# Performance work log

Measured on AMD Instinct MI355X. Metric: run time of the kernel, lower is better.

Reference implementation:

```python
import jax, jax.numpy as jnp
import numpy as np

N, E, G, H, L, GD = 100000, 1600000, 64, 128, 3, 32
NEG_SLOPE = 0.2
EPS = 1e-5


def setup_inputs() -> dict:
    key = jax.random.key(0)
    ks = jax.random.split(key, 10)
    s = 1.0 / np.sqrt(H)
    return {
        "x": jax.random.normal(ks[0], (N, H), jnp.float32),
        "global_feat": jax.random.normal(ks[1], (G, GD), jnp.float32),
        "W_src": jax.random.normal(ks[2], (L, H, H), jnp.float32) * s,
        "W_dst": jax.random.normal(ks[3], (L, H, H), jnp.float32) * s,
        "att": jax.random.normal(ks[4], (L, H), jnp.float32) * s,
        "b_conv": jnp.zeros((L, H), jnp.float32),
        "gn_w": jnp.ones((L, H), jnp.float32),
        "gn_b": jnp.zeros((L, H), jnp.float32),
        "gn_ms": jnp.ones((L, H), jnp.float32),
        "W1": jax.random.normal(ks[5], (H * L + GD, H), jnp.float32) * (1.0 / np.sqrt(H * L + GD)),
        "b1": jnp.zeros((H,), jnp.float32),
        "W2": jax.random.normal(ks[6], (H, 1), jnp.float32) * s,
        "b2": jnp.zeros((1,), jnp.float32),
        "edge_index": jax.random.randint(ks[7], (2, E), 0, N, jnp.int64),
        "batch": jnp.sort(jax.random.randint(ks[8], (N,), 0, G, jnp.int64)),
    }


def reference(x, global_feat, W_src, W_dst, att, b_conv, gn_w, gn_b, gn_ms,
              W1, b1, W2, b2, edge_index, batch):
    n = x.shape[0]
    g = global_feat.shape[0]
    layers = W_src.shape[0]
    loops = jnp.arange(n, dtype=edge_index.dtype)
    src = jnp.concatenate([edge_index[0], loops])  # add_self_loops=True
    dst = jnp.concatenate([edge_index[1], loops])
    counts = jnp.maximum(
        jax.ops.segment_sum(jnp.ones((n,), x.dtype), batch, num_segments=g), 1.0)

    outs = []
    for l in range(layers):
        # --- GATv2Conv (heads=1) ---
        xl = x @ W_src[l]          # source transform [N,H]
        xr = x @ W_dst[l]          # target transform [N,H]
        e = jax.nn.leaky_relu(xl[src] + xr[dst], NEG_SLOPE) @ att[l]  # [Etot]
        emax = jax.ops.segment_max(e, dst, num_segments=n)
        ex = jnp.exp(e - emax[dst])
        denom = jax.ops.segment_sum(ex, dst, num_segments=n)
        alpha = ex / denom[dst]
        h = jax.ops.segment_sum(alpha[:, None] * xl[src], dst, num_segments=n) + b_conv[l]
        # --- GraphNorm ---
        mean = jax.ops.segment_sum(h, batch, num_segments=g) / counts[:, None]
        sub = h - gn_ms[l] * mean[batch]
        var = jax.ops.segment_sum(sub * sub, batch, num_segments=g) / counts[:, None]
        h = gn_w[l] * sub * jax.lax.rsqrt(var[batch] + EPS) + gn_b[l]
        x = jax.nn.relu(h)
        # --- global_mean_pool ---
        outs.append(jax.ops.segment_sum(x, batch, num_segments=g) / counts[:, None])

    hcat = jnp.concatenate(outs + [global_feat], axis=1)  # JK cat + global feats
    z = jax.nn.relu(hcat @ W1 + b1)  # dropout = identity (eval)
    return z @ W2 + b2
```

## Files before the change

### kernel.cpp

```cpp
#include <hip/hip_runtime.h>
#include <hip/hip_bf16.h>
#include <math.h>

#define N_    100000
#define E_    1600000
#define ETOT_ 1700000
#define G_    64
#define H_    128
#define GH_   8192
#define L_    3
#define GD_   32
#define NEG_  0.2f
#define EPS_  1e-5f

#define NBUK_ 391
#define CH_   2048
#define MCH_  782

typedef unsigned short ushort_t;
typedef unsigned int uint_t;
typedef __attribute__((ext_vector_type(4))) float f32x4;
typedef __attribute__((ext_vector_type(8))) short bf16x8;
typedef __attribute__((ext_vector_type(8))) unsigned short ushort8;

__device__ __forceinline__ ushort_t bfb(float f) {
    __hip_bfloat16 h = __float2bfloat16(f);
    return *reinterpret_cast<ushort_t*>(&h);
}
__device__ __forceinline__ float uf(ushort_t u) {
    return __uint_as_float(((uint_t)u) << 16);
}


__global__ void k_init(float* pooled, float* gsum, float* gsq, int* gstart,
                       const int* __restrict__ batch) {
    int i = blockIdx.x * 256 + threadIdx.x;
    if (i < L_ * GH_) { pooled[i] = 0.f; gsum[i] = 0.f; gsq[i] = 0.f; }
    if (i <= G_) {
        int lo = 0, hi = N_;
        while (lo < hi) { int mid = (lo + hi) >> 1; if (batch[mid] < i) lo = mid + 1; else hi = mid; }
        gstart[i] = lo;
    }
}


__global__ __launch_bounds__(256) void k_bcount(const int* __restrict__ edst, int* __restrict__ C) {
    __shared__ int hist[NBUK_];
    int t = threadIdx.x, m = blockIdx.x;
    for (int i = t; i < NBUK_; i += 256) hist[i] = 0;
    __syncthreads();
    int base = m * CH_;
#pragma unroll
    for (int j = 0; j < CH_ / 256; j++) {
        int e = base + j * 256 + t;
        if (e < E_) atomicAdd(&hist[edst[e] >> 8], 1);
    }
    __syncthreads();
    for (int i = t; i < NBUK_; i += 256) C[i * MCH_ + m] = hist[i];
}

__global__ __launch_bounds__(1024) void k_bscan(int* __restrict__ C, int* __restrict__ bucketEdges) {
    __shared__ int arr[1024];
    int b = blockIdx.x, t = threadIdx.x;
    int v = (t < MCH_) ? C[b * MCH_ + t] : 0;
    arr[t] = v;
    __syncthreads();
    for (int off = 1; off < 1024; off <<= 1) {
        int x = (t >= off) ? arr[t - off] : 0;
        __syncthreads();
        arr[t] += x;
        __syncthreads();
    }
    if (t < MCH_) C[b * MCH_ + t] = arr[t] - v;
    if (t == 1023) bucketEdges[b] = arr[1023];
}

__global__ __launch_bounds__(512) void k_bscan2(const int* __restrict__ bucketEdges,
                                                int* __restrict__ bstartE, int* __restrict__ bstartT,
                                                int* __restrict__ rowptr) {
    __shared__ int aE[512], aT[512];
    int t = threadIdx.x;
    int e = 0, tot = 0;
    if (t < NBUK_) {
        e = bucketEdges[t];
        int nib = N_ - t * 256; if (nib > 256) nib = 256;
        tot = e + nib;
    }
    aE[t] = e; aT[t] = tot;
    __syncthreads();
    for (int off = 1; off < 512; off <<= 1) {
        int xe = (t >= off) ? aE[t - off] : 0;
        int xt = (t >= off) ? aT[t - off] : 0;
        __syncthreads();
        aE[t] += xe; aT[t] += xt;
        __syncthreads();
    }
    if (t < NBUK_) { bstartE[t] = aE[t] - e; bstartT[t] = aT[t] - tot; }
    if (t == 0) rowptr[N_] = ETOT_;
}

__global__ __launch_bounds__(256) void k_bscatter(const int* __restrict__ esrc, const int* __restrict__ edst,
                                                  const int* __restrict__ C, const int* __restrict__ bstartE,
                                                  int2* __restrict__ stag) {
    __shared__ int cur[NBUK_];
    int t = threadIdx.x, m = blockIdx.x;
    for (int i = t; i < NBUK_; i += 256) cur[i] = C[i * MCH_ + m] + bstartE[i];
    __syncthreads();
    int base = m * CH_;
#pragma unroll
    for (int j = 0; j < CH_ / 256; j++) {
        int e = base + j * 256 + t;
        if (e < E_) {
            int s = esrc[e], d = edst[e];
            int pos = atomicAdd(&cur[d >> 8], 1);
            int2 p; p.x = s; p.y = d;
            stag[pos] = p;
        }
    }
}

__global__ __launch_bounds__(256) void k_bfinal(const int2* __restrict__ stag,
                                                const int* __restrict__ bucketEdges,
                                                const int* __restrict__ bstartE, const int* __restrict__ bstartT,
                                                int* __restrict__ rowptr, int* __restrict__ colarr) {
    __shared__ int deg[256];
    __shared__ int cursor[256];
    int b = blockIdx.x, t = threadIdx.x;
    int nb0 = b * 256;
    int nib = N_ - nb0; if (nib > 256) nib = 256;
    int ebeg = bstartE[b], ecnt = bucketEdges[b];
    deg[t] = (t < nib) ? 1 : 0;
    __syncthreads();
    for (int i = t; i < ecnt; i += 256) {
        int2 p = stag[ebeg + i];
        atomicAdd(&deg[p.y - nb0], 1);
    }
    __syncthreads();
    int v = deg[t];
    cursor[t] = v;
    __syncthreads();
    for (int off = 1; off < 256; off <<= 1) {
        int x = (t >= off) ? cursor[t - off] : 0;
        __syncthreads();
        cursor[t] += x;
        __syncthreads();
    }
    int excl = cursor[t] - v;
    int rowbase = bstartT[b];
    if (t < nib) {
        rowptr[nb0 + t] = rowbase + excl;
        colarr[rowbase + excl] = nb0 + t;
    }
    __syncthreads();
    cursor[t] = excl + 1;
    __syncthreads();
    for (int i = t; i < ecnt; i += 256) {
        int2 p = stag[ebeg + i];
        int pos = atomicAdd(&cursor[p.y - nb0], 1);
        colarr[rowbase + pos] = p.x;
    }
}


__global__ void k_prep_w(const float* __restrict__ Ws, const float* __restrict__ Wd,
                         ushort_t* __restrict__ Wt) {
    int i = blockIdx.x * 256 + threadIdx.x;
    if (i >= L_ * 256 * H_) return;
    int l = i >> 15;
    int r = i & 32767;
    int c = r >> 7, k = r & 127;
    float v = (c < H_) ? Ws[(size_t)l * H_ * H_ + k * H_ + c]
                       : Wd[(size_t)l * H_ * H_ + k * H_ + (c - H_)];
    Wt[i] = bfb(v);
}


template<int FIRST>
__global__ __launch_bounds__(256) void k_mfma_t(const float* __restrict__ x0,
                                                const ushort_t* __restrict__ hin,
                                                const int* __restrict__ batch,
                                                const float* __restrict__ mv,
                                                const float* __restrict__ iv,
                                                const float* __restrict__ bb,
                                                const ushort_t* __restrict__ Wt,
                                                ushort_t* __restrict__ xlb,
                                                ushort_t* __restrict__ xrb) {
    int wv = threadIdx.x >> 6, lane = threadIdx.x & 63;
    int row0 = (blockIdx.x * 4 + wv) * 16;
    if (row0 >= N_) return;
    int sl = lane & 15, q = lane >> 4;
    int row = row0 + sl;

    bf16x8 a[4];
    if (FIRST) {
        const float* ap = x0 + (size_t)row * H_ + q * 8;
#pragma unroll
        for (int kk = 0; kk < 4; kk++) {
            float4 v0 = *(const float4*)(ap + kk * 32);
            float4 v1 = *(const float4*)(ap + kk * 32 + 4);
            bf16x8 t;
            t[0] = (short)bfb(v0.x); t[1] = (short)bfb(v0.y);
            t[2] = (short)bfb(v0.z); t[3] = (short)bfb(v0.w);
            t[4] = (short)bfb(v1.x); t[5] = (short)bfb(v1.y);
            t[6] = (short)bfb(v1.z); t[7] = (short)bfb(v1.w);
            a[kk] = t;
        }
    } else {
        int g = batch[row];
        const ushort_t* hp = hin + (size_t)row * H_ + q * 8;
        const float* mvp = mv + g * H_ + q * 8;
        const float* ivp = iv + g * H_ + q * 8;
        const float* bbp = bb + q * 8;
#pragma unroll
        for (int kk = 0; kk < 4; kk++) {
            ushort8 u = *(const ushort8*)(hp + kk * 32);
            float4 m0 = *(const float4*)(mvp + kk * 32);
            float4 m1 = *(const float4*)(mvp + kk * 32 + 4);
            float4 i0 = *(const float4*)(ivp + kk * 32);
            float4 i1 = *(const float4*)(ivp + kk * 32 + 4);
            float4 c0 = *(const float4*)(bbp + kk * 32);
            float4 c1 = *(const float4*)(bbp + kk * 32 + 4);
            bf16x8 t;
            t[0] = (short)bfb(fmaxf((uf(u[0]) - m0.x) * i0.x + c0.x, 0.f));
            t[1] = (short)bfb(fmaxf((uf(u[1]) - m0.y) * i0.y + c0.y, 0.f));
            t[2] = (short)bfb(fmaxf((uf(u[2]) - m0.z) * i0.z + c0.z, 0.f));
            t[3] = (short)bfb(fmaxf((uf(u[3]) - m0.w) * i0.w + c0.w, 0.f));
            t[4] = (short)bfb(fmaxf((uf(u[4]) - m1.x) * i1.x + c1.x, 0.f));
            t[5] = (short)bfb(fmaxf((uf(u[5]) - m1.y) * i1.y + c1.y, 0.f));
            t[6] = (short)bfb(fmaxf((uf(u[6]) - m1.z) * i1.z + c1.z, 0.f));
            t[7] = (short)bfb(fmaxf((uf(u[7]) - m1.w) * i1.w + c1.w, 0.f));
            a[kk] = t;
        }
    }

    f32x4 acc[16];
#pragma unroll
    for (int c = 0; c < 16; c++) acc[c] = (f32x4){0.f, 0.f, 0.f, 0.f};

#pragma unroll
    for (int c = 0; c < 16; c++) {
        const ushort_t* bp = Wt + (size_t)(c * 16 + sl) * H_ + q * 8;
#pragma unroll
        for (int kk = 0; kk < 4; kk++) {
            bf16x8 b = *(const bf16x8*)(bp + kk * 32);
            acc[c] = __builtin_amdgcn_mfma_f32_16x16x32_bf16(a[kk], b, acc[c], 0, 0, 0);
        }
    }

    int orow = row0 + q * 4;
#pragma unroll
    for (int c = 0; c < 8; c++)
#pragma unroll
        for (int j = 0; j < 4; j++)
            xlb[(size_t)(orow + j) * H_ + c * 16 + sl] = bfb(acc[c][j]);
#pragma unroll
    for (int c = 8; c < 16; c++)
#pragma unroll
        for (int j = 0; j < 4; j++)
            xrb[(size_t)(orow + j) * H_ + (c - 8) * 16 + sl] = bfb(acc[c][j]);
}


__global__ __launch_bounds__(256) void k_conv(const ushort_t* __restrict__ xlb,
                                              const ushort_t* __restrict__ xrb,
                                              const int* __restrict__ rowptr, const int* __restrict__ colarr,
                                              const float* __restrict__ attl, const float* __restrict__ bcl,
                                              ushort_t* __restrict__ h) {
    int tid = threadIdx.x;
    int lane = tid & 63, wv = tid >> 6;
    int sl = lane & 15, q = lane >> 4;
    int row = blockIdx.x * 16 + wv * 4 + q;
    int d0 = sl * 8;

    float xrv[8], av[8], av5[8];
    {
        ushort8 ux = *(const ushort8*)(xrb + (size_t)row * H_ + d0);
        float4 a0 = *(const float4*)(attl + d0);
        float4 a1 = *(const float4*)(attl + d0 + 4);
        av[0] = a0.x; av[1] = a0.y; av[2] = a0.z; av[3] = a0.w;
        av[4] = a1.x; av[5] = a1.y; av[6] = a1.z; av[7] = a1.w;
#pragma unroll
        for (int e = 0; e < 8; e++) { xrv[e] = uf(ux[e]); av5[e] = NEG_ * av[e]; }
    }

    int jb = rowptr[row];
    int n = rowptr[row + 1] - jb;
    int last = n - 1;

    float ssum = 0.f;
    float ac[8] = {0.f, 0.f, 0.f, 0.f, 0.f, 0.f, 0.f, 0.f};

    int c0 = colarr[jb];
    int c1 = colarr[jb + (1 < last ? 1 : last)];
    int sc = colarr[jb + (2 < last ? 2 : last)];
    ushort8 u0 = *(const ushort8*)(xlb + (size_t)c0 * H_ + d0);
    ushort8 u1 = *(const ushort8*)(xlb + (size_t)c1 * H_ + d0);

    for (int i = 0; i < n; i++) {
        int i3 = i + 3; if (i3 > last) i3 = last;
        int cn = colarr[jb + i3];
        ushort8 u2 = *(const ushort8*)(xlb + (size_t)sc * H_ + d0);

        float v[8];
        float p = 0.f;
#pragma unroll
        for (int e = 0; e < 8; e++) {
            v[e] = uf(u0[e]);
            float t = v[e] + xrv[e];
            p = fmaf(t, (t > 0.f ? av[e] : av5[e]), p);
        }
        p += __shfl_xor(p, 8);
        p += __shfl_xor(p, 4);
        p += __shfl_xor(p, 2);
        p += __shfl_xor(p, 1);
        float wgt = __expf(p);
        ssum += wgt;
#pragma unroll
        for (int e = 0; e < 8; e++) ac[e] = fmaf(wgt, v[e], ac[e]);

        u0 = u1; u1 = u2; sc = cn;
    }

    float inv = 1.f / ssum;
    float4 b0 = *(const float4*)(bcl + d0);
    float4 b1 = *(const float4*)(bcl + d0 + 4);
    ushort8 ho;
    ho[0] = bfb(ac[0] * inv + b0.x); ho[1] = bfb(ac[1] * inv + b0.y);
    ho[2] = bfb(ac[2] * inv + b0.z); ho[3] = bfb(ac[3] * inv + b0.w);
    ho[4] = bfb(ac[4] * inv + b1.x); ho[5] = bfb(ac[5] * inv + b1.y);
    ho[6] = bfb(ac[6] * inv + b1.z); ho[7] = bfb(ac[7] * inv + b1.w);
    *(ushort8*)(h + (size_t)row * H_ + d0) = ho;
}


__global__ void k_gn_stat(const ushort_t* __restrict__ h, const int* __restrict__ batch,
                          float* gsum, float* gsq) {
    int tid = threadIdx.x;
    int nb = blockIdx.x * 64;
    int d2 = (tid & 63) * 2, hh = tid >> 6;
    int nend = nb + 64; if (nend > N_) nend = N_;
    float s10 = 0.f, s11 = 0.f, s20 = 0.f, s21 = 0.f; int curg = -1;
    for (int n = nb + hh; n < nend; n += 4) {
        int g = batch[n];
        if (g != curg) {
            if (curg >= 0) {
                atomicAdd(&gsum[curg * H_ + d2], s10);
                atomicAdd(&gsum[curg * H_ + d2 + 1], s11);
                atomicAdd(&gsq[curg * H_ + d2], s20);
                atomicAdd(&gsq[curg * H_ + d2 + 1], s21);
            }
            s10 = s11 = s20 = s21 = 0.f; curg = g;
        }
        uint_t u = *(const uint_t*)(h + (size_t)n * H_ + d2);
        float v0 = __uint_as_float(u << 16);
        float v1 = __uint_as_float(u & 0xffff0000u);
        s10 += v0; s11 += v1; s20 += v0 * v0; s21 += v1 * v1;
    }
    if (curg >= 0) {
        atomicAdd(&gsum[curg * H_ + d2], s10);
        atomicAdd(&gsum[curg * H_ + d2 + 1], s11);
        atomicAdd(&gsq[curg * H_ + d2], s20);
        atomicAdd(&gsq[curg * H_ + d2 + 1], s21);
    }
}


__global__ void k_gn_fin(float* gsum, float* gsq, const int* __restrict__ gstart,
                         const float* __restrict__ gnwl, const float* __restrict__ gnmsl) {
    int i = blockIdx.x * 256 + threadIdx.x;
    if (i < GH_) {
        int g = i >> 7, d = i & 127;
        int c = gstart[g + 1] - gstart[g]; if (c < 1) c = 1;
        float ic = 1.f / (float)c;
        float mean = gsum[i] * ic;
        float e2   = gsq[i] * ic;
        float ms = gnmsl[d];
        float var = e2 - ms * (2.f - ms) * mean * mean;
        gsum[i] = ms * mean;
        gsq[i]  = gnwl[d] * rsqrtf(var + EPS_);
    }
}


__global__ void k_pool(const ushort_t* __restrict__ h, const int* __restrict__ batch,
                       const float* __restrict__ mv, const float* __restrict__ iv,
                       const float* __restrict__ bb, float* __restrict__ pooled_l) {
    int tid = threadIdx.x;
    int nb = blockIdx.x * 64;
    int d2 = (tid & 63) * 2, hh = tid >> 6;
    int nend = nb + 64; if (nend > N_) nend = N_;
    float b0 = bb[d2], b1 = bb[d2 + 1];
    float p0 = 0.f, p1 = 0.f; int curg = -1;
    float m0 = 0.f, m1 = 0.f, i0 = 0.f, i1 = 0.f;
    for (int n = nb + hh; n < nend; n += 4) {
        int g = batch[n];
        if (g != curg) {
            if (curg >= 0) {
                atomicAdd(&pooled_l[curg * H_ + d2], p0);
                atomicAdd(&pooled_l[curg * H_ + d2 + 1], p1);
            }
            p0 = 0.f; p1 = 0.f; curg = g;
            m0 = mv[g * H_ + d2]; m1 = mv[g * H_ + d2 + 1];
            i0 = iv[g * H_ + d2]; i1 = iv[g * H_ + d2 + 1];
        }
        uint_t u = *(const uint_t*)(h + (size_t)n * H_ + d2);
        float v0 = __uint_as_float(u << 16);
        float v1 = __uint_as_float(u & 0xffff0000u);
        v0 = fmaxf((v0 - m0) * i0 + b0, 0.f);
        v1 = fmaxf((v1 - m1) * i1 + b1, 0.f);
        p0 += v0; p1 += v1;
    }
    if (curg >= 0) {
        atomicAdd(&pooled_l[curg * H_ + d2], p0);
        atomicAdd(&pooled_l[curg * H_ + d2 + 1], p1);
    }
}


__global__ __launch_bounds__(128) void k_mlp(const float* __restrict__ pooled, const float* __restrict__ gfeat,
                                             const int* __restrict__ gstart,
                                             const float* __restrict__ W1, const float* __restrict__ b1,
                                             const float* __restrict__ W2, const float* __restrict__ b2,
                                             float* __restrict__ out) {
    int g = blockIdx.x;
    int c = threadIdx.x;
    __shared__ float hc[H_ * L_ + GD_];
    __shared__ float zz[H_];
    int cn = gstart[g + 1] - gstart[g]; if (cn < 1) cn = 1;
    float ic = 1.f / (float)cn;
    for (int k = c; k < H_ * L_; k += 128)
        hc[k] = pooled[(k >> 7) * GH_ + g * H_ + (k & 127)] * ic;
    if (c < GD_) hc[H_ * L_ + c] = gfeat[g * GD_ + c];
    __syncthreads();
    float z = b1[c];
#pragma unroll 4
    for (int k = 0; k < H_ * L_ + GD_; k++)
        z += hc[k] * W1[k * H_ + c];
    z = fmaxf(z, 0.f);
    zz[c] = z * W2[c];
    __syncthreads();
    for (int off = 64; off > 0; off >>= 1) {
        if (c < off) zz[c] += zz[c + off];
        __syncthreads();
    }
    if (c == 0) out[g] = zz[0] + b2[0];
}


extern "C" void kernel_launch(void* const* d_in, const int* in_sizes, int n_in,
                              void* d_out, int out_size, void* d_ws, size_t ws_size,
                              hipStream_t stream) {
    const float* x0    = (const float*)d_in[0];
    const float* gfeat = (const float*)d_in[1];
    const float* Wsrc  = (const float*)d_in[2];
    const float* Wdst  = (const float*)d_in[3];
    const float* att   = (const float*)d_in[4];
    const float* bconv = (const float*)d_in[5];
    const float* gnw   = (const float*)d_in[6];
    const float* gnb   = (const float*)d_in[7];
    const float* gnms  = (const float*)d_in[8];
    const float* W1    = (const float*)d_in[9];
    const float* b1    = (const float*)d_in[10];
    const float* W2    = (const float*)d_in[11];
    const float* b2    = (const float*)d_in[12];
    const int*   eidx  = (const int*)d_in[13];
    const int*   batch = (const int*)d_in[14];
    const int* esrc = eidx;
    const int* edst = eidx + E_;
    float* out = (float*)d_out;

    char* w = (char*)d_ws;
    size_t off = 0;
    auto alloc = [&](size_t bytes) { char* p = w + off; off += (bytes + 255) & ~(size_t)255; return p; };
    ushort_t* xlb  = (ushort_t*)alloc((size_t)N_ * H_ * 2);
    ushort_t* xrb  = (ushort_t*)alloc((size_t)N_ * H_ * 2);
    ushort_t* h    = (ushort_t*)alloc((size_t)N_ * H_ * 2);
    ushort_t* Wt   = (ushort_t*)alloc((size_t)L_ * 256 * H_ * 2);
    int*   rowptr  = (int*)alloc((size_t)(N_ + 1) * 4);
    int*   colarr  = (int*)alloc((size_t)ETOT_ * 4);
    int*   bktE    = (int*)alloc(NBUK_ * 4);
    int*   bstartE = (int*)alloc(NBUK_ * 4);
    int*   bstartT = (int*)alloc(NBUK_ * 4);
    int*   gstart  = (int*)alloc((G_ + 1) * 4);
    float* gsum    = (float*)alloc((size_t)L_ * GH_ * 4);
    float* gsq     = (float*)alloc((size_t)L_ * GH_ * 4);
    float* pooled  = (float*)alloc((size_t)L_ * GH_ * 4);
    int2* stag = (int2*)xlb;
    int*  C    = (int*)xrb;
    (void)ws_size; (void)in_sizes; (void)n_in; (void)out_size;

    k_init<<<(N_ + 255) / 256, 256, 0, stream>>>(pooled, gsum, gsq, gstart, batch);
    k_bcount<<<MCH_, 256, 0, stream>>>(edst, C);
    k_bscan<<<NBUK_, 1024, 0, stream>>>(C, bktE);
    k_bscan2<<<1, 512, 0, stream>>>(bktE, bstartE, bstartT, rowptr);
    k_bscatter<<<MCH_, 256, 0, stream>>>(esrc, edst, C, bstartE, stag);
    k_bfinal<<<NBUK_, 256, 0, stream>>>(stag, bktE, bstartE, bstartT, rowptr, colarr);
    k_prep_w<<<(L_ * 256 * H_ + 255) / 256, 256, 0, stream>>>(Wsrc, Wdst, Wt);

    int mfma_grid = (N_ / 16 + 3) / 4;
    for (int l = 0; l < L_; l++) {
        if (l == 0)
            k_mfma_t<1><<<mfma_grid, 256, 0, stream>>>(x0, h, batch, gsum, gsq, gnb,
                                                       Wt, xlb, xrb);
        else
            k_mfma_t<0><<<mfma_grid, 256, 0, stream>>>(x0, h, batch,
                                                       gsum + (size_t)(l - 1) * GH_,
                                                       gsq + (size_t)(l - 1) * GH_,
                                                       gnb + (size_t)(l - 1) * H_,
                                                       Wt + (size_t)l * 256 * H_, xlb, xrb);
        k_conv<<<N_ / 16, 256, 0, stream>>>(xlb, xrb, rowptr, colarr,
                                            att + (size_t)l * H_, bconv + (size_t)l * H_, h);
        k_gn_stat<<<(N_ + 63) / 64, 256, 0, stream>>>(h, batch,
                                                      gsum + (size_t)l * GH_, gsq + (size_t)l * GH_);
        k_gn_fin<<<GH_ / 256, 256, 0, stream>>>(gsum + (size_t)l * GH_, gsq + (size_t)l * GH_,
                                                gstart, gnw + (size_t)l * H_, gnms + (size_t)l * H_);
        k_pool<<<(N_ + 63) / 64, 256, 0, stream>>>(h, batch,
                                                   gsum + (size_t)l * GH_, gsq + (size_t)l * GH_,
                                                   gnb + (size_t)l * H_, pooled + (size_t)l * GH_);
    }

    k_mlp<<<G_, 128, 0, stream>>>(pooled, gfeat, gstart, W1, b1, W2, b2, out);
}
```

Before: 630.6 us.

## Sort conv rows by degree, pack staging edges, fuse weight prep into init

Adds a degree histogram, scan and scatter that build a degree-sorted permutation of destination nodes. k_conv then walks rows in that order, so each wave handles rows of similar edge count and waits less on its longest row. Edge staging is packed into one 32-bit word (source shifted, low byte of destination), halving staging traffic. The weight bf16 transpose is folded into k_init, and the conv gather loop becomes a two-way unrolled prefetch. The trade-offs are two extra small launches and scattered, non-contiguous row reads and writes of xrb and h inside k_conv.

```diff
diff --git a/kernel.cpp b/kernel.cpp
--- a/kernel.cpp
+++ b/kernel.cpp
@@ -16,6 +16,7 @@
 #define NBUK_ 391
 #define CH_   2048
 #define MCH_  782
+#define DBINS 1024
 
 typedef unsigned short ushort_t;
 typedef unsigned int uint_t;
@@ -32,14 +33,25 @@
 }
 
 
-__global__ void k_init(float* pooled, float* gsum, float* gsq, int* gstart,
-                       const int* __restrict__ batch) {
+__global__ void k_init(float* pooled, float* gsum, float* gsq, int* gstart, int* dcnt,
+                       const int* __restrict__ batch,
+                       const float* __restrict__ Ws, const float* __restrict__ Wd,
+                       ushort_t* __restrict__ Wt) {
     int i = blockIdx.x * 256 + threadIdx.x;
     if (i < L_ * GH_) { pooled[i] = 0.f; gsum[i] = 0.f; gsq[i] = 0.f; }
+    if (i < DBINS) dcnt[i] = 0;
     if (i <= G_) {
         int lo = 0, hi = N_;
         while (lo < hi) { int mid = (lo + hi) >> 1; if (batch[mid] < i) lo = mid + 1; else hi = mid; }
         gstart[i] = lo;
+    }
+    if (i < L_ * 256 * H_) {
+        int l = i >> 15;
+        int r = i & 32767;
+        int c = r >> 7, k = r & 127;
+        float v = (c < H_) ? Ws[(size_t)l * H_ * H_ + k * H_ + c]
+                           : Wd[(size_t)l * H_ * H_ + k * H_ + (c - H_)];
+        Wt[i] = bfb(v);
     }
 }
 
@@ -101,7 +113,7 @@
 
 __global__ __launch_bounds__(256) void k_bscatter(const int* __restrict__ esrc, const int* __restrict__ edst,
                                                   const int* __restrict__ C, const int* __restrict__ bstartE,
-                                                  int2* __restrict__ stag) {
+                                                  uint_t* __restrict__ stag) {
     __shared__ int cur[NBUK_];
     int t = threadIdx.x, m = blockIdx.x;
     for (int i = t; i < NBUK_; i += 256) cur[i] = C[i * MCH_ + m] + bstartE[i];
@@ -113,16 +125,16 @@
         if (e < E_) {
             int s = esrc[e], d = edst[e];
             int pos = atomicAdd(&cur[d >> 8], 1);
-            int2 p; p.x = s; p.y = d;
-            stag[pos] = p;
-        }
-    }
-}
-
-__global__ __launch_bounds__(256) void k_bfinal(const int2* __restrict__ stag,
+            stag[pos] = ((uint_t)s << 8) | (uint_t)(d & 255);
+        }
+    }
+}
+
+__global__ __launch_bounds__(256) void k_bfinal(const uint_t* __restrict__ stag,
                                                 const int* __restrict__ bucketEdges,
                                                 const int* __restrict__ bstartE, const int* __restrict__ bstartT,
-                                                int* __restrict__ rowptr, int* __restrict__ colarr) {
+                                                int* __restrict__ rowptr, int* __restrict__ colarr,
+                                                int* __restrict__ dcnt) {
     __shared__ int deg[256];
     __shared__ int cursor[256];
     int b = blockIdx.x, t = threadIdx.x;
@@ -132,8 +144,8 @@
     deg[t] = (t < nib) ? 1 : 0;
     __syncthreads();
     for (int i = t; i < ecnt; i += 256) {
-        int2 p = stag[ebeg + i];
-        atomicAdd(&deg[p.y - nb0], 1);
+        uint_t p = stag[ebeg + i];
+        atomicAdd(&deg[p & 255u], 1);
     }
     __syncthreads();
     int v = deg[t];
@@ -150,28 +162,46 @@
     if (t < nib) {
         rowptr[nb0 + t] = rowbase + excl;
         colarr[rowbase + excl] = nb0 + t;
+        int d = v; if (d > DBINS - 1) d = DBINS - 1;
+        atomicAdd(&dcnt[d], 1);
     }
     __syncthreads();
     cursor[t] = excl + 1;
     __syncthreads();
     for (int i = t; i < ecnt; i += 256) {
-        int2 p = stag[ebeg + i];
-        int pos = atomicAdd(&cursor[p.y - nb0], 1);
-        colarr[rowbase + pos] = p.x;
-    }
-}
-
-
-__global__ void k_prep_w(const float* __restrict__ Ws, const float* __restrict__ Wd,
-                         ushort_t* __restrict__ Wt) {
+        uint_t p = stag[ebeg + i];
+        int pos = atomicAdd(&cursor[p & 255u], 1);
+        colarr[rowbase + pos] = (int)(p >> 8);
+    }
+}
+
+
+__global__ __launch_bounds__(1024) void k_degscan(int* __restrict__ dcnt) {
+    __shared__ int arr[1024];
+    int t = threadIdx.x;
+    int v = dcnt[t];
+    arr[t] = v;
+    __syncthreads();
+    for (int off = 1; off < 1024; off <<= 1) {
+        int x = (t >= off) ? arr[t - off] : 0;
+        __syncthreads();
+        arr[t] += x;
+        __syncthreads();
+    }
+    dcnt[t] = arr[t] - v;
+}
+
+__global__ void k_degscatter(const int* __restrict__ rowptr, int* __restrict__ dcnt,
+                             int* __restrict__ perm, int* __restrict__ jbarr, int* __restrict__ narr) {
     int i = blockIdx.x * 256 + threadIdx.x;
-    if (i >= L_ * 256 * H_) return;
-    int l = i >> 15;
-    int r = i & 32767;
-    int c = r >> 7, k = r & 127;
-    float v = (c < H_) ? Ws[(size_t)l * H_ * H_ + k * H_ + c]
-                       : Wd[(size_t)l * H_ * H_ + k * H_ + (c - H_)];
-    Wt[i] = bfb(v);
+    if (i >= N_) return;
+    int jb = rowptr[i];
+    int n = rowptr[i + 1] - jb;
+    int d = n > DBINS - 1 ? DBINS - 1 : n;
+    int slot = atomicAdd(&dcnt[d], 1);
+    perm[slot] = i;
+    jbarr[slot] = jb;
+    narr[slot] = n;
 }
 
 
@@ -263,18 +293,22 @@
 
 __global__ __launch_bounds__(256) void k_conv(const ushort_t* __restrict__ xlb,
                                               const ushort_t* __restrict__ xrb,
-                                              const int* __restrict__ rowptr, const int* __restrict__ colarr,
+                                              const int* __restrict__ perm,
+                                              const int* __restrict__ jbarr,
+                                              const int* __restrict__ narr,
+                                              const int* __restrict__ colarr,
                                               const float* __restrict__ attl, const float* __restrict__ bcl,
                                               ushort_t* __restrict__ h) {
     int tid = threadIdx.x;
     int lane = tid & 63, wv = tid >> 6;
     int sl = lane & 15, q = lane >> 4;
-    int row = blockIdx.x * 16 + wv * 4 + q;
+    int slot = blockIdx.x * 16 + wv * 4 + q;
+    int prow = perm[slot];
     int d0 = sl * 8;
 
     float xrv[8], av[8], av5[8];
     {
-        ushort8 ux = *(const ushort8*)(xrb + (size_t)row * H_ + d0);
+        ushort8 ux = *(const ushort8*)(xrb + (size_t)prow * H_ + d0);
         float4 a0 = *(const float4*)(attl + d0);
         float4 a1 = *(const float4*)(attl + d0 + 4);
         av[0] = a0.x; av[1] = a0.y; av[2] = a0.z; av[3] = a0.w;
@@ -283,29 +317,18 @@
         for (int e = 0; e < 8; e++) { xrv[e] = uf(ux[e]); av5[e] = NEG_ * av[e]; }
     }
 
-    int jb = rowptr[row];
-    int n = rowptr[row + 1] - jb;
-    int last = n - 1;
+    int jb = jbarr[slot];
+    int n = narr[slot];
 
     float ssum = 0.f;
     float ac[8] = {0.f, 0.f, 0.f, 0.f, 0.f, 0.f, 0.f, 0.f};
 
-    int c0 = colarr[jb];
-    int c1 = colarr[jb + (1 < last ? 1 : last)];
-    int sc = colarr[jb + (2 < last ? 2 : last)];
-    ushort8 u0 = *(const ushort8*)(xlb + (size_t)c0 * H_ + d0);
-    ushort8 u1 = *(const ushort8*)(xlb + (size_t)c1 * H_ + d0);
-
-    for (int i = 0; i < n; i++) {
-        int i3 = i + 3; if (i3 > last) i3 = last;
-        int cn = colarr[jb + i3];
-        ushort8 u2 = *(const ushort8*)(xlb + (size_t)sc * H_ + d0);
-
+    auto PROC = [&](const ushort8& u) {
         float v[8];
         float p = 0.f;
 #pragma unroll
         for (int e = 0; e < 8; e++) {
-            v[e] = uf(u0[e]);
+            v[e] = uf(u[e]);
             float t = v[e] + xrv[e];
             p = fmaf(t, (t > 0.f ? av[e] : av5[e]), p);
         }
@@ -317,9 +340,24 @@
         ssum += wgt;
 #pragma unroll
         for (int e = 0; e < 8; e++) ac[e] = fmaf(wgt, v[e], ac[e]);
-
-        u0 = u1; u1 = u2; sc = cn;
-    }
+    };
+
+    int cA = colarr[jb];
+    ushort8 uA = *(const ushort8*)(xlb + (size_t)cA * H_ + d0);
+    int cB = colarr[jb + (n > 1 ? 1 : 0)];
+    ushort8 uB = *(const ushort8*)(xlb + (size_t)cB * H_ + d0);
+
+    int i = 0;
+    for (; i + 2 < n; i += 2) {
+        int cC = colarr[jb + i + 2];
+        int cD = colarr[jb + (i + 3 < n ? i + 3 : i + 2)];
+        PROC(uA);
+        uA = *(const ushort8*)(xlb + (size_t)cC * H_ + d0);
+        PROC(uB);
+        uB = *(const ushort8*)(xlb + (size_t)cD * H_ + d0);
+    }
+    PROC(uA);
+    if (i + 1 < n) PROC(uB);
 
     float inv = 1.f / ssum;
     float4 b0 = *(const float4*)(bcl + d0);
@@ -329,7 +367,7 @@
     ho[2] = bfb(ac[2] * inv + b0.z); ho[3] = bfb(ac[3] * inv + b0.w);
     ho[4] = bfb(ac[4] * inv + b1.x); ho[5] = bfb(ac[5] * inv + b1.y);
     ho[6] = bfb(ac[6] * inv + b1.z); ho[7] = bfb(ac[7] * inv + b1.w);
-    *(ushort8*)(h + (size_t)row * H_ + d0) = ho;
+    *(ushort8*)(h + (size_t)prow * H_ + d0) = ho;
 }
 
 
@@ -478,24 +516,30 @@
     ushort_t* Wt   = (ushort_t*)alloc((size_t)L_ * 256 * H_ * 2);
     int*   rowptr  = (int*)alloc((size_t)(N_ + 1) * 4);
     int*   colarr  = (int*)alloc((size_t)ETOT_ * 4);
+    int*   perm    = (int*)alloc((size_t)N_ * 4);
+    int*   jbarr   = (int*)alloc((size_t)N_ * 4);
+    int*   narr    = (int*)alloc((size_t)N_ * 4);
     int*   bktE    = (int*)alloc(NBUK_ * 4);
     int*   bstartE = (int*)alloc(NBUK_ * 4);
     int*   bstartT = (int*)alloc(NBUK_ * 4);
+    int*   dcnt    = (int*)alloc(DBINS * 4);
     int*   gstart  = (int*)alloc((G_ + 1) * 4);
     float* gsum    = (float*)alloc((size_t)L_ * GH_ * 4);
     float* gsq     = (float*)alloc((size_t)L_ * GH_ * 4);
     float* pooled  = (float*)alloc((size_t)L_ * GH_ * 4);
-    int2* stag = (int2*)xlb;
-    int*  C    = (int*)xrb;
+    uint_t* stag = (uint_t*)xlb;
+    int*    C    = (int*)xrb;
     (void)ws_size; (void)in_sizes; (void)n_in; (void)out_size;
 
-    k_init<<<(N_ + 255) / 256, 256, 0, stream>>>(pooled, gsum, gsq, gstart, batch);
+    k_init<<<(N_ + 255) / 256, 256, 0, stream>>>(pooled, gsum, gsq, gstart, dcnt, batch,
+                                                 Wsrc, Wdst, Wt);
     k_bcount<<<MCH_, 256, 0, stream>>>(edst, C);
     k_bscan<<<NBUK_, 1024, 0, stream>>>(C, bktE);
     k_bscan2<<<1, 512, 0, stream>>>(bktE, bstartE, bstartT, rowptr);
     k_bscatter<<<MCH_, 256, 0, stream>>>(esrc, edst, C, bstartE, stag);
-    k_bfinal<<<NBUK_, 256, 0, stream>>>(stag, bktE, bstartE, bstartT, rowptr, colarr);
-    k_prep_w<<<(L_ * 256 * H_ + 255) / 256, 256, 0, stream>>>(Wsrc, Wdst, Wt);
+    k_bfinal<<<NBUK_, 256, 0, stream>>>(stag, bktE, bstartE, bstartT, rowptr, colarr, dcnt);
+    k_degscan<<<1, 1024, 0, stream>>>(dcnt);
+    k_degscatter<<<(N_ + 255) / 256, 256, 0, stream>>>(rowptr, dcnt, perm, jbarr, narr);
 
     int mfma_grid = (N_ / 16 + 3) / 4;
     for (int l = 0; l < L_; l++) {
@@ -508,7 +552,7 @@
                                                        gsq + (size_t)(l - 1) * GH_,
                                                        gnb + (size_t)(l - 1) * H_,
                                                        Wt + (size_t)l * 256 * H_, xlb, xrb);
-        k_conv<<<N_ / 16, 256, 0, stream>>>(xlb, xrb, rowptr, colarr,
+        k_conv<<<N_ / 16, 256, 0, stream>>>(xlb, xrb, perm, jbarr, narr, colarr,
                                             att + (size_t)l * H_, bconv + (size_t)l * H_, h);
         k_gn_stat<<<(N_ + 63) / 64, 256, 0, stream>>>(h, batch,
                                                       gsum + (size_t)l * GH_, gsq + (size_t)l * GH_);
```

New measurement: 1.178 ms. 1.87x slower.
